# Optimization experiments

Measured on AMD Instinct MI355X. Metric: run time of the kernel, lower is better.

The kernel has to match this reference:

```python
import jax, jax.numpy as jnp
import numpy as np

K = 1024          # num_embeddings
D = 64            # embedding_dim
EPS = 0.05        # entropic regularization epsilon
DUAL_STEPS = 10
DUAL_LR = 0.5
TEMP = 0.5        # hist_temperature
OT_W = 1.0
CC = 0.25         # commitment cost


def _norm_prob(p):
    p = jnp.clip(p, 1e-12)
    return p / p.sum()


def _dual_obj(phi, src_w, tgt_w, cost):
    src_w = _norm_prob(src_w)
    tgt_w = _norm_prob(tgt_w)
    log_tgt = jnp.log(jnp.clip(tgt_w, 1e-12))[None, :]          # [1, K]
    lse = jax.scipy.special.logsumexp(log_tgt + (-cost + phi[None, :]) / EPS, axis=1)  # [K]
    return jnp.sum(src_w * (-EPS * lse)) + jnp.sum(tgt_w * phi)


def _dual_ot_loss(src_w, tgt_w, cost):
    src_d = jax.lax.stop_gradient(src_w)
    tgt_d = jax.lax.stop_gradient(tgt_w)
    cost_d = jax.lax.stop_gradient(cost)
    grad_phi = jax.grad(_dual_obj)
    def body(_, phi):
        return phi + DUAL_LR * grad_phi(phi, src_d, tgt_d, cost_d)
    phi = jax.lax.fori_loop(0, DUAL_STEPS, body, jnp.zeros_like(tgt_d))
    return _dual_obj(jax.lax.stop_gradient(phi), src_w, tgt_w, cost)


def _gaussian_target():
    idx = jnp.arange(K, dtype=jnp.float32)
    mean = (K - 1) / 2.0
    std = K / 6.0
    t = jnp.exp(-0.5 * ((idx - mean) / std) ** 2)
    return t / jnp.clip(t.sum(), 1e-12)


def _forward(inputs, codebook):
    B, C, H, W = inputs.shape
    x_bhwc = jnp.transpose(inputs, (0, 2, 3, 1))                 # [B,H,W,C]
    flat = x_bhwc.reshape(-1, C)                                  # [N, D]
    # squared-distance matrix [N, K]
    d = (jnp.sum(flat * flat, axis=1, keepdims=True)
         + jnp.sum(codebook * codebook, axis=1)
         - 2.0 * flat @ codebook.T)
    idx = jnp.argmin(d, axis=1)                                   # [N]
    enc = jax.nn.one_hot(idx, K, dtype=jnp.float32)               # [N, K]
    # power normalize (one-hot power = sqrt(1/K) < 1, so a no-op, but faithful)
    power = jnp.sqrt(jnp.mean(enc * enc))
    enc = jnp.where(power > 1.0, enc / power, enc)
    clean_q = enc @ codebook                                      # [N, D]
    noisy_q = clean_q                                             # channel=None -> zero noise
    # training losses
    hard_hist = jnp.mean(enc, axis=0)                             # [K]
    soft = jax.nn.softmax(-d / TEMP, axis=1)                      # [N, K]
    soft_hist = jnp.mean(soft, axis=0)
    # value = hard_hist, gradient flows via soft_hist (straight-through hist)
    cw = _norm_prob(hard_hist + soft_hist - jax.lax.stop_gradient(soft_hist))
    target = _gaussian_target()
    support = jnp.arange(K, dtype=jnp.float32)
    cost = jnp.abs(support[:, None] - support[None, :])           # cdist(p=2) on 1-d support
    ot_loss = OT_W * _dual_ot_loss(cw, target, cost)
    codebook_loss = jnp.mean((clean_q - jax.lax.stop_gradient(flat)) ** 2)
    commit_loss = jnp.mean((jax.lax.stop_gradient(clean_q) - flat) ** 2)
    loss = codebook_loss + CC * commit_loss + ot_loss
    # straight-through quantized output
    nq = noisy_q.reshape(B, H, W, C)
    quantized = x_bhwc + jax.lax.stop_gradient(nq - x_bhwc)
    quantized = jnp.transpose(quantized, (0, 3, 1, 2))            # [B,C,H,W]
    avg = jnp.mean(enc, axis=0)
    perplexity = jnp.exp(-jnp.sum(avg * jnp.log(avg + 1e-10)))
    return quantized, loss, perplexity


def setup_inputs() -> dict:
    key = jax.random.key(0)
    k1, k2 = jax.random.split(key)
    inputs = jax.random.normal(k1, (32, D, 32, 32), dtype=jnp.float32)
    codebook = jax.random.uniform(k2, (K, D), minval=-1.0 / K, maxval=1.0 / K, dtype=jnp.float32)
    return {"inputs": inputs, "codebook": codebook}


def reference(inputs, codebook):
    return _forward(inputs, codebook)
```

## Files before the change

kernel.cpp:

```cpp
#include <hip/hip_runtime.h>
#include <math.h>

#define NPTS 32768
#define KCB  1024
#define DIM  64
#define HW   1024
#define CHW  65536

typedef short  bf16x8 __attribute__((ext_vector_type(8)));
typedef float  f32x16 __attribute__((ext_vector_type(16)));

__device__ __forceinline__ unsigned short f2b_rne(float f) {
  unsigned u = __float_as_uint(f);
  unsigned r = 0x7FFFu + ((u >> 16) & 1u);
  return (unsigned short)((u + r) >> 16);
}

__device__ __forceinline__ float block_sum(float v, float* scratch) {
  #pragma unroll
  for (int o = 32; o > 0; o >>= 1) v += __shfl_down(v, o, 64);
  int wid  = threadIdx.x >> 6;
  int lane = threadIdx.x & 63;
  __syncthreads();
  if (lane == 0) scratch[wid] = v;
  __syncthreads();
  float s = 0.f;
  int nw = blockDim.x >> 6;
  for (int w = 0; w < nw; ++w) s += scratch[w];
  return s;
}

__global__ __launch_bounds__(64) void k_cvt(const float* __restrict__ cb,
                                            float4* __restrict__ cbf,
                                            float* __restrict__ cnorm,
                                            int* __restrict__ hist) {
  int c = blockIdx.x * 64 + threadIdx.x;
  hist[c] = 0;
  const float4* row4 = (const float4*)(cb + c * DIM);
  float4 r[16];
  #pragma unroll
  for (int i = 0; i < 16; ++i) r[i] = row4[i];
  float s = 0.f;
  #pragma unroll
  for (int i = 0; i < 16; ++i) {
    s = fmaf(r[i].x, r[i].x, s); s = fmaf(r[i].y, r[i].y, s);
    s = fmaf(r[i].z, r[i].z, s); s = fmaf(r[i].w, r[i].w, s);
  }
  cnorm[c] = s;
  int ch = c >> 6, nt = (c >> 5) & 1, n = c & 31;
  int base = ch * 1024 + nt * 256 + n;
  #pragma unroll
  for (int o = 0; o < 8; ++o) {
    float f[8] = {r[2*o].x, r[2*o].y, r[2*o].z, r[2*o].w,
                  r[2*o+1].x, r[2*o+1].y, r[2*o+1].z, r[2*o+1].w};
    unsigned hu[4], lu[4];
    #pragma unroll
    for (int j = 0; j < 4; ++j) {
      unsigned short h0 = f2b_rne(f[2*j]),   h1 = f2b_rne(f[2*j+1]);
      float hf0 = __uint_as_float((unsigned)h0 << 16);
      float hf1 = __uint_as_float((unsigned)h1 << 16);
      unsigned short l0 = f2b_rne(f[2*j] - hf0), l1 = f2b_rne(f[2*j+1] - hf1);
      hu[j] = (unsigned)h0 | ((unsigned)h1 << 16);
      lu[j] = (unsigned)l0 | ((unsigned)l1 << 16);
    }
    int pos = base + (o >> 1) * 64 + (o & 1) * 32;
    uint4 hv = {hu[0], hu[1], hu[2], hu[3]};
    uint4 lv = {lu[0], lu[1], lu[2], lu[3]};
    cbf[pos]       = *(float4*)&hv;
    cbf[pos + 512] = *(float4*)&lv;
  }
}

__global__ __launch_bounds__(256, 2) void k_dist(const float* __restrict__ x,
                                                 const float* __restrict__ cb,
                                                 const float4* __restrict__ cbf,
                                                 const float* __restrict__ cnorm,
                                                 int* __restrict__ hist,
                                                 float* __restrict__ msep,
                                                 float* __restrict__ out) {
  __shared__ unsigned short lph[64][72], lpl[64][72];
  __shared__ float s_cn[KCB];
  __shared__ float s_sx[64], s_part[4][64];
  __shared__ unsigned long long s_pk[64][2];
  __shared__ int   s_bd[64];
  __shared__ float scratch[4];

  int tid = threadIdx.x;
  int t   = blockIdx.x;
  int n0  = t * 64;
  int b   = n0 >> 10;
  int hw0 = n0 & 1023;

  *(float4*)&s_cn[tid * 4] = *(const float4*)(cnorm + tid * 4);

  float fx[16];
  {
    int p = tid & 63, q4 = tid >> 6;
    const float* xb = x + b * CHW + hw0 + p;
    float s = 0.f;
    unsigned short hb[16], lb[16];
    #pragma unroll
    for (int i = 0; i < 16; ++i) {
      int c = q4 * 16 + i;
      float f = xb[c * HW];
      fx[i] = f;
      s = fmaf(f, f, s);
      unsigned short h = f2b_rne(f);
      float hf = __uint_as_float(((unsigned)h) << 16);
      hb[i] = h;
      lb[i] = f2b_rne(f - hf);
    }
    s_part[q4][p] = s;
    #pragma unroll
    for (int j = 0; j < 8; ++j) {
      *(unsigned*)&lph[p][q4 * 16 + 2 * j] = (unsigned)hb[2*j] | ((unsigned)hb[2*j+1] << 16);
      *(unsigned*)&lpl[p][q4 * 16 + 2 * j] = (unsigned)lb[2*j] | ((unsigned)lb[2*j+1] << 16);
    }
  }
  __syncthreads();
  if (tid < 64)
    s_sx[tid] = ((s_part[0][tid] + s_part[1][tid]) + s_part[2][tid]) + s_part[3][tid];
  __syncthreads();

  int w = tid >> 6, l = tid & 63;
  int wm = w >> 1, wn = w & 1;
  int u = l >> 5, n = l & 31;

  bf16x8 ah[4], al[4];
  {
    int pt = wm * 32 + n;
    #pragma unroll
    for (int s = 0; s < 4; ++s) {
      ah[s] = *(const bf16x8*)&lph[pt][(2 * s + u) * 8];
      al[s] = *(const bf16x8*)&lpl[pt][(2 * s + u) * 8];
    }
  }
  float sxr[16];
  #pragma unroll
  for (int r = 0; r < 16; ++r)
    sxr[r] = s_sx[wm * 32 + (r & 3) + 8 * (r >> 2) + 4 * u];

  float best[16]; int bidx[16];
  #pragma unroll
  for (int r = 0; r < 16; ++r) { best[r] = 3.4e38f; bidx[r] = 0; }

  int bofs = wn * 256 + u * 32 + n;
  const bf16x8* gb = (const bf16x8*)cbf;

  bf16x8 cbh[4], cbl[4], nbh[4], nbl[4];
  #pragma unroll
  for (int s = 0; s < 4; ++s) {
    cbh[s] = gb[bofs + s * 64];
    cbl[s] = gb[bofs + s * 64 + 512];
  }

  #pragma unroll
  for (int ch = 0; ch < 16; ++ch) {
    if (ch < 15) {
      const bf16x8* gn = gb + (ch + 1) * 1024;
      #pragma unroll
      for (int s = 0; s < 4; ++s) {
        nbh[s] = gn[bofs + s * 64];
        nbl[s] = gn[bofs + s * 64 + 512];
      }
    }
    f32x16 acc;
    #pragma unroll
    for (int r = 0; r < 16; ++r) acc[r] = 0.f;
    #pragma unroll
    for (int s = 0; s < 4; ++s) {
      acc = __builtin_amdgcn_mfma_f32_32x32x16_bf16(ah[s], cbh[s], acc, 0, 0, 0);
      acc = __builtin_amdgcn_mfma_f32_32x32x16_bf16(ah[s], cbl[s], acc, 0, 0, 0);
      acc = __builtin_amdgcn_mfma_f32_32x32x16_bf16(al[s], cbh[s], acc, 0, 0, 0);
    }
    int   kk  = ch * 64 + wn * 32 + n;
    float cnv = s_cn[kk];
    #pragma unroll
    for (int r = 0; r < 16; ++r) {
      float dist = (sxr[r] + cnv) - 2.0f * acc[r];
      if (dist < best[r]) { best[r] = dist; bidx[r] = kk; }
    }
    if (ch < 15) {
      #pragma unroll
      for (int s = 0; s < 4; ++s) { cbh[s] = nbh[s]; cbl[s] = nbl[s]; }
    }
  }

  #pragma unroll
  for (int r = 0; r < 16; ++r) {
    unsigned long long p =
        ((unsigned long long)__float_as_uint(best[r]) << 32) | (unsigned)bidx[r];
    #pragma unroll
    for (int m = 1; m < 32; m <<= 1) {
      unsigned long long o = __shfl_xor(p, m, 64);
      p = (o < p) ? o : p;
    }
    if (n == 0)
      s_pk[wm * 32 + (r & 3) + 8 * (r >> 2) + 4 * u][wn] = p;
  }
  __syncthreads();
  if (tid < 64) {
    unsigned long long a = s_pk[tid][0], c2 = s_pk[tid][1];
    unsigned long long mn = (c2 < a) ? c2 : a;
    int bd = (int)(mn & 0xffffffffull);
    s_bd[tid] = bd;
    atomicAdd(&hist[bd], 1);
  }
  __syncthreads();

  float se = 0.f;
  {
    int p = tid & 63, cg = tid >> 6;
    int bd = s_bd[p];
    const float* crow = cb + bd * DIM;
    float* ob = out + b * CHW + hw0 + p;
    #pragma unroll 4
    for (int i = 0; i < 16; ++i) {
      int c = cg * 16 + i;
      float xv   = fx[i];
      float diff = crow[c] - xv;
      se += diff * diff;
      ob[c * HW] = xv + diff;
    }
  }
  float tot = block_sum(se, scratch);
  if (tid == 0) msep[t] = tot;
}

__global__ __launch_bounds__(256) void k_ot(const int* __restrict__ hist,
                                            const float* __restrict__ msep,
                                            float* __restrict__ out) {
  __shared__ __align__(16) float s_lt[KCB + 8], s_src[KCB + 8],
                                 s_phi[KCB + 8], s_lse[KCB + 8];
  __shared__ float scratch[4];
  int tid = threadIdx.x;
  int i0  = tid * 4;
  int sl0 = i0 + 4;

  float msetot = block_sum(msep[tid] + msep[tid + 256], scratch);

  int4 hi4 = *(const int4*)(hist + i0);
  int  hi[4] = {hi4.x, hi4.y, hi4.z, hi4.w};
  float tj[4], hj[4];
  #pragma unroll
  for (int j = 0; j < 4; ++j) {
    float fi = (float)(i0 + j);
    float zz = (fi - 511.5f) / (1024.0f / 6.0f);
    tj[j] = expf(-0.5f * zz * zz);
    hj[j] = (float)hi[j] * (1.0f / 32768.0f);
  }
  float St = block_sum(tj[0] + tj[1] + tj[2] + tj[3], scratch);
  float tgt[4], ltw[4];
  float l2 = 0.f;
  #pragma unroll
  for (int j = 0; j < 4; ++j) { tgt[j] = fmaxf(tj[j] / fmaxf(St, 1e-12f), 1e-12f); l2 += tgt[j]; }
  float St2 = block_sum(l2, scratch);
  #pragma unroll
  for (int j = 0; j < 4; ++j) { tgt[j] = tgt[j] / St2; ltw[j] = logf(fmaxf(tgt[j], 1e-12f)); }

  float m1[4], srcw[4];
  float l3 = 0.f;
  #pragma unroll
  for (int j = 0; j < 4; ++j) { m1[j] = fmaxf(hj[j], 1e-12f); l3 += m1[j]; }
  float S1 = block_sum(l3, scratch);
  float l4 = 0.f;
  #pragma unroll
  for (int j = 0; j < 4; ++j) { srcw[j] = fmaxf(m1[j] / S1, 1e-12f); l4 += srcw[j]; }
  float S2 = block_sum(l4, scratch);
  float l5 = 0.f;
  #pragma unroll
  for (int j = 0; j < 4; ++j) { srcw[j] = srcw[j] / S2; l5 += hj[j] * logf(hj[j] + 1e-10f); }
  float ent = block_sum(l5, scratch);

  *(float4*)&s_lt[sl0]  = *(float4*)ltw;
  *(float4*)&s_src[sl0] = *(float4*)srcw;
  *(float4*)&s_phi[sl0] = make_float4(0.f, 0.f, 0.f, 0.f);
  *(float4*)&s_lse[sl0] = make_float4(0.f, 0.f, 0.f, 0.f);
  if (tid == 0) {
    #pragma unroll
    for (int p = 0; p < 4; ++p) {
      s_lt[p] = -100.f; s_src[p] = 0.f; s_phi[p] = 0.f; s_lse[p] = 0.f;
      s_lt[KCB+4+p] = -100.f; s_src[KCB+4+p] = 0.f; s_phi[KCB+4+p] = 0.f; s_lse[KCB+4+p] = 0.f;
    }
  }
  __syncthreads();

  float ws[12];
  #pragma unroll
  for (int m = 0; m < 3; ++m) *(float4*)&ws[m*4] = *(float4*)&s_src[i0 + m*4];

  float phi[4] = {0.f, 0.f, 0.f, 0.f};
  float lse[4];
  for (int it = 0; it <= 10; ++it) {
    float wl[12], wp[12];
    #pragma unroll
    for (int m = 0; m < 3; ++m) {
      *(float4*)&wl[m*4] = *(float4*)&s_lt[i0 + m*4];
      *(float4*)&wp[m*4] = *(float4*)&s_phi[i0 + m*4];
    }
    #pragma unroll
    for (int j = 0; j < 4; ++j) {
      float mx = -3.0e38f;
      float vv[5];
      #pragma unroll
      for (int qq = 0; qq < 5; ++qq) {
        int m = j + qq + 2;
        float a = wl[m] + (wp[m] - fabsf((float)(qq - 2))) * 20.0f;
        vv[qq] = a;
        mx = fmaxf(mx, a);
      }
      float ssum = 0.f;
      #pragma unroll
      for (int qq = 0; qq < 5; ++qq) ssum += expf(vv[qq] - mx);
      lse[j] = mx + logf(ssum);
    }
    *(float4*)&s_lse[sl0] = *(float4*)lse;
    __syncthreads();
    if (it == 10) break;

    float we[12];
    #pragma unroll
    for (int m = 0; m < 3; ++m) *(float4*)&we[m*4] = *(float4*)&s_lse[i0 + m*4];
    #pragma unroll
    for (int j = 0; j < 4; ++j) {
      float basej = ltw[j] + phi[j] * 20.0f;
      float cs = 0.f;
      #pragma unroll
      for (int qq = 0; qq < 5; ++qq) {
        int m = j + qq + 2;
        float a = basej - fabsf((float)(qq - 2)) * 20.0f;
        cs += ws[m] * expf(a - we[m]);
      }
      phi[j] += 0.5f * (tgt[j] - cs);
    }
    *(float4*)&s_phi[sl0] = *(float4*)phi;
    __syncthreads();
  }

  float lo = 0.f;
  #pragma unroll
  for (int j = 0; j < 4; ++j) lo += srcw[j] * (-0.05f * lse[j]) + tgt[j] * phi[j];
  float ot = block_sum(lo, scratch);

  if (tid == 0) {
    out[2097152] = 1.25f * (msetot * (1.0f / 2097152.0f)) + ot;
    out[2097153] = expf(-ent);
  }
}

extern "C" void kernel_launch(void* const* d_in, const int* in_sizes, int n_in,
                              void* d_out, int out_size, void* d_ws, size_t ws_size,
                              hipStream_t stream) {
  const float* x  = (const float*)d_in[0];
  const float* cb = (const float*)d_in[1];
  float* out = (float*)d_out;

  float4* cbf  = (float4*)d_ws;
  float*  cnorm = (float*)((char*)d_ws + 262144);
  int*    hist  = (int*)((char*)d_ws + 266240);
  float*  msep  = (float*)((char*)d_ws + 270336);

  k_cvt<<<16, 64, 0, stream>>>(cb, cbf, cnorm, hist);
  k_dist<<<512, 256, 0, stream>>>(x, cb, cbf, cnorm, hist, msep, out);
  k_ot<<<1, 256, 0, stream>>>(hist, msep, out);
}
```

Measured before the change: 109.0 us.

## Split codebook search across two blocks per tile and fuse OT into last block

Each 64-point tile is now handled by two blocks, each scanning half the codebook. Partial argmin results go to global memory, and an atomic ticket lets the second block to finish merge them, then do the histogram and writeback. The separate OT kernel is folded into the last finishing block through a done counter, with shared memory reused via a union. This doubles the grid to 1024 blocks to fill more CUs and removes one kernel launch, at the cost of extra global traffic, fences, and re-reading x in the writeback.

```diff
diff --git a/kernel.cpp b/kernel.cpp
--- a/kernel.cpp
+++ b/kernel.cpp
@@ -33,9 +33,13 @@
 __global__ __launch_bounds__(64) void k_cvt(const float* __restrict__ cb,
                                             float4* __restrict__ cbf,
                                             float* __restrict__ cnorm,
-                                            int* __restrict__ hist) {
+                                            int* __restrict__ hist,
+                                            int* __restrict__ ticket,
+                                            int* __restrict__ done2) {
   int c = blockIdx.x * 64 + threadIdx.x;
   hist[c] = 0;
+  if (c < 512) ticket[c] = 0;
+  if (c == 0)  *done2 = 0;
   const float4* row4 = (const float4*)(cb + c * DIM);
   float4 r[16];
   #pragma unroll
@@ -77,23 +81,36 @@
                                                  const float* __restrict__ cnorm,
                                                  int* __restrict__ hist,
                                                  float* __restrict__ msep,
+                                                 unsigned long long* __restrict__ gpm,
+                                                 int* __restrict__ ticket,
+                                                 int* __restrict__ done2,
                                                  float* __restrict__ out) {
-  __shared__ unsigned short lph[64][72], lpl[64][72];
-  __shared__ float s_cn[KCB];
+  __shared__ __align__(16) union SM {
+    struct {
+      unsigned short lph[64][72];
+      unsigned short lpl[64][72];
+      float cn[KCB];
+    } g;
+    struct {
+      float lt[KCB + 8]; float src[KCB + 8]; float phi[KCB + 8]; float lse[KCB + 8];
+    } o;
+  } sm;
   __shared__ float s_sx[64], s_part[4][64];
   __shared__ unsigned long long s_pk[64][2];
   __shared__ int   s_bd[64];
   __shared__ float scratch[4];
+  __shared__ int   s_flag;
 
   int tid = threadIdx.x;
-  int t   = blockIdx.x;
+  int g   = blockIdx.x;
+  int h   = g >> 9;
+  int t   = g & 511;
   int n0  = t * 64;
   int b   = n0 >> 10;
   int hw0 = n0 & 1023;
 
-  *(float4*)&s_cn[tid * 4] = *(const float4*)(cnorm + tid * 4);
-
-  float fx[16];
+  *(float4*)&sm.g.cn[tid * 4] = *(const float4*)(cnorm + tid * 4);
+
   {
     int p = tid & 63, q4 = tid >> 6;
     const float* xb = x + b * CHW + hw0 + p;
@@ -103,18 +120,17 @@
     for (int i = 0; i < 16; ++i) {
       int c = q4 * 16 + i;
       float f = xb[c * HW];
-      fx[i] = f;
       s = fmaf(f, f, s);
-      unsigned short h = f2b_rne(f);
-      float hf = __uint_as_float(((unsigned)h) << 16);
-      hb[i] = h;
+      unsigned short hs = f2b_rne(f);
+      float hf = __uint_as_float(((unsigned)hs) << 16);
+      hb[i] = hs;
       lb[i] = f2b_rne(f - hf);
     }
     s_part[q4][p] = s;
     #pragma unroll
     for (int j = 0; j < 8; ++j) {
-      *(unsigned*)&lph[p][q4 * 16 + 2 * j] = (unsigned)hb[2*j] | ((unsigned)hb[2*j+1] << 16);
-      *(unsigned*)&lpl[p][q4 * 16 + 2 * j] = (unsigned)lb[2*j] | ((unsigned)lb[2*j+1] << 16);
+      *(unsigned*)&sm.g.lph[p][q4 * 16 + 2 * j] = (unsigned)hb[2*j] | ((unsigned)hb[2*j+1] << 16);
+      *(unsigned*)&sm.g.lpl[p][q4 * 16 + 2 * j] = (unsigned)lb[2*j] | ((unsigned)lb[2*j+1] << 16);
     }
   }
   __syncthreads();
@@ -131,8 +147,8 @@
     int pt = wm * 32 + n;
     #pragma unroll
     for (int s = 0; s < 4; ++s) {
-      ah[s] = *(const bf16x8*)&lph[pt][(2 * s + u) * 8];
-      al[s] = *(const bf16x8*)&lpl[pt][(2 * s + u) * 8];
+      ah[s] = *(const bf16x8*)&sm.g.lph[pt][(2 * s + u) * 8];
+      al[s] = *(const bf16x8*)&sm.g.lpl[pt][(2 * s + u) * 8];
     }
   }
   float sxr[16];
@@ -148,16 +164,20 @@
   const bf16x8* gb = (const bf16x8*)cbf;
 
   bf16x8 cbh[4], cbl[4], nbh[4], nbl[4];
-  #pragma unroll
-  for (int s = 0; s < 4; ++s) {
-    cbh[s] = gb[bofs + s * 64];
-    cbl[s] = gb[bofs + s * 64 + 512];
-  }
-
-  #pragma unroll
-  for (int ch = 0; ch < 16; ++ch) {
-    if (ch < 15) {
-      const bf16x8* gn = gb + (ch + 1) * 1024;
+  {
+    const bf16x8* g0 = gb + (h * 8) * 1024;
+    #pragma unroll
+    for (int s = 0; s < 4; ++s) {
+      cbh[s] = g0[bofs + s * 64];
+      cbl[s] = g0[bofs + s * 64 + 512];
+    }
+  }
+
+  #pragma unroll
+  for (int chl = 0; chl < 8; ++chl) {
+    int gc = h * 8 + chl;
+    if (chl < 7) {
+      const bf16x8* gn = gb + (gc + 1) * 1024;
       #pragma unroll
       for (int s = 0; s < 4; ++s) {
         nbh[s] = gn[bofs + s * 64];
@@ -173,14 +193,14 @@
       acc = __builtin_amdgcn_mfma_f32_32x32x16_bf16(ah[s], cbl[s], acc, 0, 0, 0);
       acc = __builtin_amdgcn_mfma_f32_32x32x16_bf16(al[s], cbh[s], acc, 0, 0, 0);
     }
-    int   kk  = ch * 64 + wn * 32 + n;
-    float cnv = s_cn[kk];
+    int   kk  = gc * 64 + wn * 32 + n;
+    float cnv = sm.g.cn[kk];
     #pragma unroll
     for (int r = 0; r < 16; ++r) {
       float dist = (sxr[r] + cnv) - 2.0f * acc[r];
       if (dist < best[r]) { best[r] = dist; bidx[r] = kk; }
     }
-    if (ch < 15) {
+    if (chl < 7) {
       #pragma unroll
       for (int s = 0; s < 4; ++s) { cbh[s] = nbh[s]; cbl[s] = nbl[s]; }
     }
@@ -199,9 +219,22 @@
       s_pk[wm * 32 + (r & 3) + 8 * (r >> 2) + 4 * u][wn] = p;
   }
   __syncthreads();
+
+  unsigned long long hm = 0ull;
   if (tid < 64) {
     unsigned long long a = s_pk[tid][0], c2 = s_pk[tid][1];
-    unsigned long long mn = (c2 < a) ? c2 : a;
+    hm = (c2 < a) ? c2 : a;
+    gpm[(unsigned)g * 64 + tid] = hm;
+  }
+  __syncthreads();
+  if (tid == 0) { __threadfence(); s_flag = atomicAdd(&ticket[t], 1); }
+  __syncthreads();
+  if (s_flag == 0) return;
+
+  __threadfence();
+  if (tid < 64) {
+    unsigned long long other = gpm[((unsigned)(1 - h) * 512 + (unsigned)t) * 64 + tid];
+    unsigned long long mn = (other < hm) ? other : hm;
     int bd = (int)(mn & 0xffffffffull);
     s_bd[tid] = bd;
     atomicAdd(&hist[bd], 1);
@@ -213,11 +246,12 @@
     int p = tid & 63, cg = tid >> 6;
     int bd = s_bd[p];
     const float* crow = cb + bd * DIM;
+    const float* xp = x + b * CHW + hw0 + p;
     float* ob = out + b * CHW + hw0 + p;
     #pragma unroll 4
     for (int i = 0; i < 16; ++i) {
       int c = cg * 16 + i;
-      float xv   = fx[i];
+      float xv   = xp[c * HW];
       float diff = crow[c] - xv;
       se += diff * diff;
       ob[c * HW] = xv + diff;
@@ -225,126 +259,127 @@
   }
   float tot = block_sum(se, scratch);
   if (tid == 0) msep[t] = tot;
-}
-
-__global__ __launch_bounds__(256) void k_ot(const int* __restrict__ hist,
-                                            const float* __restrict__ msep,
-                                            float* __restrict__ out) {
-  __shared__ __align__(16) float s_lt[KCB + 8], s_src[KCB + 8],
-                                 s_phi[KCB + 8], s_lse[KCB + 8];
-  __shared__ float scratch[4];
-  int tid = threadIdx.x;
-  int i0  = tid * 4;
-  int sl0 = i0 + 4;
-
-  float msetot = block_sum(msep[tid] + msep[tid + 256], scratch);
-
-  int4 hi4 = *(const int4*)(hist + i0);
-  int  hi[4] = {hi4.x, hi4.y, hi4.z, hi4.w};
-  float tj[4], hj[4];
-  #pragma unroll
-  for (int j = 0; j < 4; ++j) {
-    float fi = (float)(i0 + j);
-    float zz = (fi - 511.5f) / (1024.0f / 6.0f);
-    tj[j] = expf(-0.5f * zz * zz);
-    hj[j] = (float)hi[j] * (1.0f / 32768.0f);
-  }
-  float St = block_sum(tj[0] + tj[1] + tj[2] + tj[3], scratch);
-  float tgt[4], ltw[4];
-  float l2 = 0.f;
-  #pragma unroll
-  for (int j = 0; j < 4; ++j) { tgt[j] = fmaxf(tj[j] / fmaxf(St, 1e-12f), 1e-12f); l2 += tgt[j]; }
-  float St2 = block_sum(l2, scratch);
-  #pragma unroll
-  for (int j = 0; j < 4; ++j) { tgt[j] = tgt[j] / St2; ltw[j] = logf(fmaxf(tgt[j], 1e-12f)); }
-
-  float m1[4], srcw[4];
-  float l3 = 0.f;
-  #pragma unroll
-  for (int j = 0; j < 4; ++j) { m1[j] = fmaxf(hj[j], 1e-12f); l3 += m1[j]; }
-  float S1 = block_sum(l3, scratch);
-  float l4 = 0.f;
-  #pragma unroll
-  for (int j = 0; j < 4; ++j) { srcw[j] = fmaxf(m1[j] / S1, 1e-12f); l4 += srcw[j]; }
-  float S2 = block_sum(l4, scratch);
-  float l5 = 0.f;
-  #pragma unroll
-  for (int j = 0; j < 4; ++j) { srcw[j] = srcw[j] / S2; l5 += hj[j] * logf(hj[j] + 1e-10f); }
-  float ent = block_sum(l5, scratch);
-
-  *(float4*)&s_lt[sl0]  = *(float4*)ltw;
-  *(float4*)&s_src[sl0] = *(float4*)srcw;
-  *(float4*)&s_phi[sl0] = make_float4(0.f, 0.f, 0.f, 0.f);
-  *(float4*)&s_lse[sl0] = make_float4(0.f, 0.f, 0.f, 0.f);
-  if (tid == 0) {
-    #pragma unroll
-    for (int p = 0; p < 4; ++p) {
-      s_lt[p] = -100.f; s_src[p] = 0.f; s_phi[p] = 0.f; s_lse[p] = 0.f;
-      s_lt[KCB+4+p] = -100.f; s_src[KCB+4+p] = 0.f; s_phi[KCB+4+p] = 0.f; s_lse[KCB+4+p] = 0.f;
-    }
-  }
-  __syncthreads();
-
-  float ws[12];
-  #pragma unroll
-  for (int m = 0; m < 3; ++m) *(float4*)&ws[m*4] = *(float4*)&s_src[i0 + m*4];
-
-  float phi[4] = {0.f, 0.f, 0.f, 0.f};
-  float lse[4];
-  for (int it = 0; it <= 10; ++it) {
-    float wl[12], wp[12];
-    #pragma unroll
-    for (int m = 0; m < 3; ++m) {
-      *(float4*)&wl[m*4] = *(float4*)&s_lt[i0 + m*4];
-      *(float4*)&wp[m*4] = *(float4*)&s_phi[i0 + m*4];
-    }
+
+  __syncthreads();
+  if (tid == 0) { __threadfence(); s_flag = atomicAdd(done2, 1); }
+  __syncthreads();
+  if (s_flag != 511) return;
+  __threadfence();
+
+  {
+    int i0  = tid * 4;
+    int sl0 = i0 + 4;
+
+    float msetot = block_sum(msep[tid] + msep[tid + 256], scratch);
+
+    int4 hi4 = *(const int4*)(hist + i0);
+    int  hi[4] = {hi4.x, hi4.y, hi4.z, hi4.w};
+    float tj[4], hj[4];
     #pragma unroll
     for (int j = 0; j < 4; ++j) {
-      float mx = -3.0e38f;
-      float vv[5];
-      #pragma unroll
-      for (int qq = 0; qq < 5; ++qq) {
-        int m = j + qq + 2;
-        float a = wl[m] + (wp[m] - fabsf((float)(qq - 2))) * 20.0f;
-        vv[qq] = a;
-        mx = fmaxf(mx, a);
+      float fi = (float)(i0 + j);
+      float zz = (fi - 511.5f) / (1024.0f / 6.0f);
+      tj[j] = expf(-0.5f * zz * zz);
+      hj[j] = (float)hi[j] * (1.0f / 32768.0f);
+    }
+    float St = block_sum(tj[0] + tj[1] + tj[2] + tj[3], scratch);
+    float tgt[4], ltw[4];
+    float l2 = 0.f;
+    #pragma unroll
+    for (int j = 0; j < 4; ++j) { tgt[j] = fmaxf(tj[j] / fmaxf(St, 1e-12f), 1e-12f); l2 += tgt[j]; }
+    float St2 = block_sum(l2, scratch);
+    #pragma unroll
+    for (int j = 0; j < 4; ++j) { tgt[j] = tgt[j] / St2; ltw[j] = logf(fmaxf(tgt[j], 1e-12f)); }
+
+    float m1[4], srcw[4];
+    float l3 = 0.f;
+    #pragma unroll
+    for (int j = 0; j < 4; ++j) { m1[j] = fmaxf(hj[j], 1e-12f); l3 += m1[j]; }
+    float S1 = block_sum(l3, scratch);
+    float l4 = 0.f;
+    #pragma unroll
+    for (int j = 0; j < 4; ++j) { srcw[j] = fmaxf(m1[j] / S1, 1e-12f); l4 += srcw[j]; }
+    float S2 = block_sum(l4, scratch);
+    float l5 = 0.f;
+    #pragma unroll
+    for (int j = 0; j < 4; ++j) { srcw[j] = srcw[j] / S2; l5 += hj[j] * logf(hj[j] + 1e-10f); }
+    float ent = block_sum(l5, scratch);
+
+    *(float4*)&sm.o.lt[sl0]  = *(float4*)ltw;
+    *(float4*)&sm.o.src[sl0] = *(float4*)srcw;
+    *(float4*)&sm.o.phi[sl0] = make_float4(0.f, 0.f, 0.f, 0.f);
+    *(float4*)&sm.o.lse[sl0] = make_float4(0.f, 0.f, 0.f, 0.f);
+    if (tid == 0) {
+      #pragma unroll
+      for (int p = 0; p < 4; ++p) {
+        sm.o.lt[p] = -100.f; sm.o.src[p] = 0.f; sm.o.phi[p] = 0.f; sm.o.lse[p] = 0.f;
+        sm.o.lt[KCB+4+p] = -100.f; sm.o.src[KCB+4+p] = 0.f;
+        sm.o.phi[KCB+4+p] = 0.f;   sm.o.lse[KCB+4+p] = 0.f;
       }
-      float ssum = 0.f;
-      #pragma unroll
-      for (int qq = 0; qq < 5; ++qq) ssum += expf(vv[qq] - mx);
-      lse[j] = mx + logf(ssum);
-    }
-    *(float4*)&s_lse[sl0] = *(float4*)lse;
+    }
     __syncthreads();
-    if (it == 10) break;
-
-    float we[12];
-    #pragma unroll
-    for (int m = 0; m < 3; ++m) *(float4*)&we[m*4] = *(float4*)&s_lse[i0 + m*4];
-    #pragma unroll
-    for (int j = 0; j < 4; ++j) {
-      float basej = ltw[j] + phi[j] * 20.0f;
-      float cs = 0.f;
-      #pragma unroll
-      for (int qq = 0; qq < 5; ++qq) {
-        int m = j + qq + 2;
-        float a = basej - fabsf((float)(qq - 2)) * 20.0f;
-        cs += ws[m] * expf(a - we[m]);
+
+    float ws[12];
+    #pragma unroll
+    for (int m = 0; m < 3; ++m) *(float4*)&ws[m*4] = *(float4*)&sm.o.src[i0 + m*4];
+
+    float phi[4] = {0.f, 0.f, 0.f, 0.f};
+    float lse[4];
+    for (int it = 0; it <= 10; ++it) {
+      float wl[12], wp[12];
+      #pragma unroll
+      for (int m = 0; m < 3; ++m) {
+        *(float4*)&wl[m*4] = *(float4*)&sm.o.lt[i0 + m*4];
+        *(float4*)&wp[m*4] = *(float4*)&sm.o.phi[i0 + m*4];
       }
-      phi[j] += 0.5f * (tgt[j] - cs);
-    }
-    *(float4*)&s_phi[sl0] = *(float4*)phi;
-    __syncthreads();
-  }
-
-  float lo = 0.f;
-  #pragma unroll
-  for (int j = 0; j < 4; ++j) lo += srcw[j] * (-0.05f * lse[j]) + tgt[j] * phi[j];
-  float ot = block_sum(lo, scratch);
-
-  if (tid == 0) {
-    out[2097152] = 1.25f * (msetot * (1.0f / 2097152.0f)) + ot;
-    out[2097153] = expf(-ent);
+      #pragma unroll
+      for (int j = 0; j < 4; ++j) {
+        float mx = -3.0e38f;
+        float vv[5];
+        #pragma unroll
+        for (int qq = 0; qq < 5; ++qq) {
+          int m = j + qq + 2;
+          float a = wl[m] + (wp[m] - fabsf((float)(qq - 2))) * 20.0f;
+          vv[qq] = a;
+          mx = fmaxf(mx, a);
+        }
+        float ssum = 0.f;
+        #pragma unroll
+        for (int qq = 0; qq < 5; ++qq) ssum += expf(vv[qq] - mx);
+        lse[j] = mx + logf(ssum);
+      }
+      *(float4*)&sm.o.lse[sl0] = *(float4*)lse;
+      __syncthreads();
+      if (it == 10) break;
+
+      float we[12];
+      #pragma unroll
+      for (int m = 0; m < 3; ++m) *(float4*)&we[m*4] = *(float4*)&sm.o.lse[i0 + m*4];
+      #pragma unroll
+      for (int j = 0; j < 4; ++j) {
+        float basej = ltw[j] + phi[j] * 20.0f;
+        float cs = 0.f;
+        #pragma unroll
+        for (int qq = 0; qq < 5; ++qq) {
+          int m = j + qq + 2;
+          float a = basej - fabsf((float)(qq - 2)) * 20.0f;
+          cs += ws[m] * expf(a - we[m]);
+        }
+        phi[j] += 0.5f * (tgt[j] - cs);
+      }
+      *(float4*)&sm.o.phi[sl0] = *(float4*)phi;
+      __syncthreads();
+    }
+
+    float lo = 0.f;
+    #pragma unroll
+    for (int j = 0; j < 4; ++j) lo += srcw[j] * (-0.05f * lse[j]) + tgt[j] * phi[j];
+    float ot = block_sum(lo, scratch);
+
+    if (tid == 0) {
+      out[2097152] = 1.25f * (msetot * (1.0f / 2097152.0f)) + ot;
+      out[2097153] = expf(-ent);
+    }
   }
 }
 
@@ -359,8 +394,11 @@
   float*  cnorm = (float*)((char*)d_ws + 262144);
   int*    hist  = (int*)((char*)d_ws + 266240);
   float*  msep  = (float*)((char*)d_ws + 270336);
-
-  k_cvt<<<16, 64, 0, stream>>>(cb, cbf, cnorm, hist);
-  k_dist<<<512, 256, 0, stream>>>(x, cb, cbf, cnorm, hist, msep, out);
-  k_ot<<<1, 256, 0, stream>>>(hist, msep, out);
+  int*    ticket = (int*)((char*)d_ws + 272384);
+  int*    done2  = (int*)((char*)d_ws + 274432);
+  unsigned long long* gpm = (unsigned long long*)((char*)d_ws + 274496);
+
+  k_cvt<<<16, 64, 0, stream>>>(cb, cbf, cnorm, hist, ticket, done2);
+  k_dist<<<1024, 256, 0, stream>>>(x, cb, cbf, cnorm, hist, msep,
+                                   gpm, ticket, done2, out);
 }
```

Measured after the change: 188.7 us. 73.1% more time.
